# Kernel tuning notes

Hardware: AMD Instinct MI355X
Metric: run time of the kernel (lower is better)

The kernel has to match this reference:

```python
import jax, jax.numpy as jnp
import numpy as np

B = 16      # number of graphs (equal-sized, batch = repeat(arange(B), N))


def _knn_edges(pos, k, total):
    """Batch-aware kNN graph, torch_geometric knn_graph semantics.

    loop=False, flow='source_to_target': for each query node i, its k nearest
    neighbors j produce edges (row=j neighbor/source, col=i query/target).
    Returns (row, col) as flat global int32 index arrays of length B*N*k.
    """
    N = total // B
    posb = pos.reshape(B, N, -1)                      # [B, N, 3]
    sq = jnp.sum(posb * posb, axis=-1)                # [B, N]
    # squared Euclidean distances, [B, N, N]
    d2 = sq[:, :, None] + sq[:, None, :] - 2.0 * jnp.einsum('bnd,bmd->bnm', posb, posb)
    d2 = jnp.where(jnp.eye(N, dtype=bool)[None], jnp.inf, d2)  # exclude self-loops
    _, nbr = jax.lax.top_k(-d2, k)                    # [B, N, k] local neighbor idx
    offs = (jnp.arange(B, dtype=nbr.dtype) * N)[:, None, None]
    row = (nbr + offs).reshape(-1)                                      # neighbors (sources)
    col = jnp.broadcast_to(jnp.arange(N, dtype=nbr.dtype)[None, :, None] + offs,
                           (B, N, k)).reshape(-1)                       # query nodes (targets)
    return row, col


def reference(x, pos, batch, k):
    total = x.shape[0]
    row, col = _knn_edges(pos, k, total)
    # scatter_mean(x[col], row, dim_size=total): mean of gathered features per row index
    sums = jax.ops.segment_sum(x[col], row, num_segments=total)          # [total, d]
    cnt = jax.ops.segment_sum(jnp.ones(row.shape, x.dtype), row, num_segments=total)
    x_neigh_mean = sums / jnp.maximum(cnt, 1.0)[:, None]                 # empty rows -> 0
    return jnp.sum(jnp.abs(x - x_neigh_mean), axis=-1)                   # L1 norm, [total]


def setup_inputs() -> dict:
    key = jax.random.key(0)
    k1, k2 = jax.random.split(key)
    N = 4096
    x = jax.random.normal(k1, (B * N, 64), dtype=jnp.float32)
    pos = jax.random.normal(k2, (B * N, 3), dtype=jnp.float32)
    batch = jnp.repeat(jnp.arange(B, dtype=jnp.int64), N)
    return {"x": x, "pos": pos, "batch": batch, "k": 10}
```

## Files before the change

### kernel.cpp

```cpp
#include <hip/hip_runtime.h>
#include <stdint.h>

#define NB 16
#define NN 4096
#define KK 10
#define NL 11
#define FD 64
#define TOTAL (NB * NN)
#define NW 8
#define CH 512
#define SOCT 32
#define QG 64
#define PCAP 64
#define PPITCH 129

typedef float f2 __attribute__((ext_vector_type(2)));

#define INFF __int_as_float(0x7f800000)

__device__ __forceinline__ f2 d2pair(f2 nmx, f2 nmy, f2 nmz, f2 sqi2,
                                     float4 A, float4 B) {
#pragma clang fp contract(off)
    f2 cx = {A.x, A.y}, cy = {A.z, A.w};
    f2 cz = {B.x, B.y}, cw = {B.z, B.w};
    f2 t = nmx * cx + nmy * cy;
    f2 nd = t + nmz * cz;
    nd = nd + nd;
    f2 s = sqi2 + cw;
    return s + nd;
}

__device__ __forceinline__ uint32_t d2exact(float mx, float my, float mz, float sqi,
                                            float cx, float cy, float cz, float cw) {
    float dot = __fadd_rn(__fadd_rn(__fmul_rn(mx, cx), __fmul_rn(my, cy)),
                          __fmul_rn(mz, cz));
    float d2 = __fsub_rn(__fadd_rn(sqi, cw), __fmul_rn(2.0f, dot));
    return __float_as_uint(d2);
}

__global__ __launch_bounds__(256) void prep_kernel(const float* __restrict__ pos,
                                                   float4* __restrict__ pp4,
                                                   int* __restrict__ cnt) {
    const int p = blockIdx.x * 256 + threadIdx.x;
    const float* s = pos + (size_t)p * 6;
    float x0 = s[0], y0 = s[1], z0 = s[2];
    float x1 = s[3], y1 = s[4], z1 = s[5];
    float q0 = __fadd_rn(__fadd_rn(__fmul_rn(x0, x0), __fmul_rn(y0, y0)),
                         __fmul_rn(z0, z0));
    float q1 = __fadd_rn(__fadd_rn(__fmul_rn(x1, x1), __fmul_rn(y1, y1)),
                         __fmul_rn(z1, z1));
    pp4[2 * p + 0] = make_float4(x0, x1, y0, y1);
    pp4[2 * p + 1] = make_float4(z0, z1, q0, q1);
    cnt[2 * p + 0] = 0;
    cnt[2 * p + 1] = 0;
}

__global__ __launch_bounds__(512, 8) void knn_kernel(const float4* __restrict__ pp4,
                                                     int* __restrict__ cnt,
                                                     int* __restrict__ colfix,
                                                     int* __restrict__ nbr) {
    __shared__ uint32_t pool[QG * PPITCH];
    __shared__ float tau_s[QG];
    __shared__ unsigned int qcnt[QG];
    float* poolf = (float*)pool;

    const int tid = threadIdx.x;
    const int lane = tid & 63;
    const int w = __builtin_amdgcn_readfirstlane(tid >> 6);
    const int batch = blockIdx.x >> 6;
    const int qloc = ((blockIdx.x & 63) << 6) | lane;
    const int gbase = batch << 12;
    const int gq = gbase + qloc;

    float4 mA = pp4[(gq >> 1) * 2 + 0];
    float4 mB = pp4[(gq >> 1) * 2 + 1];
    const bool hi = (qloc & 1);
    const float mx = hi ? mA.y : mA.x;
    const float my = hi ? mA.w : mA.z;
    const float mz = hi ? mB.y : mB.x;
    const float sqi = hi ? mB.w : mB.z;
    const f2 nmx = {-mx, -mx}, nmy = {-my, -my}, nmz = {-mz, -mz};
    const f2 sqi2 = {sqi, sqi};

    const float4* __restrict__ cp = pp4 + (size_t)(gbase + w * CH);

    float L[NL];
#pragma unroll
    for (int t = 0; t < NL; t++) L[t] = INFF;

#pragma unroll 2
    for (int o = 0; o < SOCT; ++o) {
        const float4* cb = cp + o * 8;
        f2 d0 = d2pair(nmx, nmy, nmz, sqi2, cb[0], cb[1]);
        f2 d1 = d2pair(nmx, nmy, nmz, sqi2, cb[2], cb[3]);
        f2 d2v = d2pair(nmx, nmy, nmz, sqi2, cb[4], cb[5]);
        f2 d3 = d2pair(nmx, nmy, nmz, sqi2, cb[6], cb[7]);
        float m0 = fminf(d0.x, d0.y), m1 = fminf(d1.x, d1.y);
        float m2 = fminf(d2v.x, d2v.y), m3 = fminf(d3.x, d3.y);
        float m = fminf(fminf(m0, m1), fminf(m2, m3));
#pragma unroll
        for (int t = 0; t < NL - 1; ++t) L[t] = __builtin_amdgcn_fmed3f(L[t], L[t + 1], m);
        L[NL - 1] = fminf(L[NL - 1], m);
    }
#pragma unroll
    for (int t = 0; t < NL; t++) poolf[tid * NL + t] = L[t];
    if (tid < QG) qcnt[tid] = 0u;
    __syncthreads();

    if (tid < QG) {
        int p[NW];
#pragma unroll
        for (int u = 0; u < NW; u++) p[u] = NL - 1;
        float tau = INFF;
        for (int it = 0; it < NL; ++it) {
            float best = INFF;
            int bw = 0;
#pragma unroll
            for (int u = 0; u < NW; u++) {
                float v = (p[u] >= 0) ? poolf[(u * QG + tid) * NL + p[u]] : INFF;
                if (v < best) { best = v; bw = u; }
            }
            p[bw]--;
            tau = best;
        }
        tau_s[tid] = tau;
    }
    __syncthreads();

    const float tau = tau_s[lane];
#pragma unroll 2
    for (int pi = 0; pi < CH / 2; ++pi) {
        f2 d = d2pair(nmx, nmy, nmz, sqi2, cp[2 * pi], cp[2 * pi + 1]);
        if (fminf(d.x, d.y) <= tau) {
            if (d.x <= tau) {
                unsigned pp = atomicAdd(&qcnt[lane], 1u);
                if (pp < PCAP) pool[lane * PPITCH + 2 * pp + 1] = (uint32_t)(w * CH + 2 * pi);
            }
            if (d.y <= tau) {
                unsigned pp = atomicAdd(&qcnt[lane], 1u);
                if (pp < PCAP) pool[lane * PPITCH + 2 * pp + 1] = (uint32_t)(w * CH + 2 * pi + 1);
            }
        }
    }
    __syncthreads();

    if (tid < QG) {
        uint64_t S[KK];
#pragma unroll
        for (int t = 0; t < KK; t++) S[t] = ~0ull;
        unsigned R = qcnt[tid];
        if (R > PCAP) R = PCAP;
        for (unsigned e = 0; e < R; ++e) {
            uint32_t ix = pool[tid * PPITCH + 2 * e + 1];
            if (ix == (uint32_t)qloc) continue;
            int g = gbase + (int)ix;
            float4 A = pp4[(g >> 1) * 2 + 0];
            float4 B = pp4[(g >> 1) * 2 + 1];
            bool ch = (ix & 1);
            uint32_t db = d2exact(mx, my, mz, sqi,
                                  ch ? A.y : A.x, ch ? A.w : A.z,
                                  ch ? B.y : B.x, ch ? B.w : B.z);
            uint64_t k64 = ((uint64_t)db << 32) | ix;
            if (k64 < S[0]) {
                bool sh[KK];
                sh[0] = true;
#pragma unroll
                for (int t = 1; t < KK; t++) sh[t] = (k64 < S[t]);
#pragma unroll
                for (int t = 0; t < KK; t++) {
                    uint64_t vac = sh[t] ? k64 : S[t];
                    S[t] = (t + 1 < KK) ? (sh[t + 1] ? S[t + 1] : vac) : vac;
                }
            }
        }
#pragma unroll
        for (int t = 0; t < KK; t++) {
            int jl = (int)(S[t] & 0xffffffffu);
            int gj = gbase + jl;
            int p = atomicAdd(&cnt[gj], 1);
            if (colfix) {
                if (p < 64) colfix[(gj << 6) | p] = gq;
            } else {
                nbr[gq * KK + t] = gj;
            }
        }
    }
}

__global__ __launch_bounds__(256) void out_bucket_kernel(const float4* __restrict__ x4,
                                                         const int* __restrict__ colfix,
                                                         const int* __restrict__ cnt,
                                                         float* __restrict__ out) {
    const int gid = blockIdx.x * 256 + threadIdx.x;
    const int n = gid >> 4;
    const int s = gid & 15;
    const int c = cnt[n];
    const int cc = (c > 64) ? 64 : c;
    const int base = n << 6;
    float4 acc = make_float4(0.f, 0.f, 0.f, 0.f);
    int e = 0;
    for (; e + 2 <= cc; e += 2) {
        int q0 = colfix[base + e], q1 = colfix[base + e + 1];
        float4 v0 = x4[(q0 << 4) | s];
        float4 v1 = x4[(q1 << 4) | s];
        acc.x += v0.x; acc.y += v0.y; acc.z += v0.z; acc.w += v0.w;
        acc.x += v1.x; acc.y += v1.y; acc.z += v1.z; acc.w += v1.w;
    }
    if (e < cc) {
        int q0 = colfix[base + e];
        float4 v0 = x4[(q0 << 4) | s];
        acc.x += v0.x; acc.y += v0.y; acc.z += v0.z; acc.w += v0.w;
    }
    const float inv = 1.0f / (float)(c > 1 ? c : 1);
    float4 mn = x4[(n << 4) | s];
    float v = fabsf(mn.x - acc.x * inv) + fabsf(mn.y - acc.y * inv) +
              fabsf(mn.z - acc.z * inv) + fabsf(mn.w - acc.w * inv);
    v += __shfl_xor(v, 1, 64);
    v += __shfl_xor(v, 2, 64);
    v += __shfl_xor(v, 4, 64);
    v += __shfl_xor(v, 8, 64);
    if (s == 0) out[n] = v;
}

__global__ __launch_bounds__(1024) void scan_kernel(const int* __restrict__ cnt,
                                                    int* __restrict__ offs) {
    __shared__ int lds[1024];
    const int t = threadIdx.x;
    const int base = t * 64;
    int s = 0;
    for (int i = 0; i < 64; i++) s += cnt[base + i];
    lds[t] = s;
    __syncthreads();
    for (int off = 1; off < 1024; off <<= 1) {
        int v = (t >= off) ? lds[t - off] : 0;
        __syncthreads();
        lds[t] += v;
        __syncthreads();
    }
    int run = lds[t] - s;
    for (int i = 0; i < 64; i++) {
        offs[base + i] = run;
        run += cnt[base + i];
    }
}

__global__ __launch_bounds__(256) void fill_kernel(const int* __restrict__ nbr,
                                                   int* __restrict__ offs,
                                                   int* __restrict__ col) {
    const int i = blockIdx.x * 256 + threadIdx.x;
#pragma unroll
    for (int t = 0; t < KK; t++) {
        int j = nbr[i * KK + t];
        int p = atomicAdd(&offs[j], 1);
        col[p] = i;
    }
}

__global__ __launch_bounds__(256) void out_kernel(const float* __restrict__ x,
                                                  const int* __restrict__ col,
                                                  const int* __restrict__ offs_end,
                                                  const int* __restrict__ cnt,
                                                  float* __restrict__ out) {
    const int gtid = blockIdx.x * 256 + threadIdx.x;
    const int n = gtid >> 6;
    const int lane = gtid & 63;
    const int c = cnt[n];
    const int end = offs_end[n];
    const int start = end - c;
    float s = 0.0f;
    for (int e = start; e < end; e++) {
        int i = col[e];
        s += x[(size_t)i * FD + lane];
    }
    float mean = s / (float)(c > 1 ? c : 1);
    float v = fabsf(x[(size_t)n * FD + lane] - mean);
#pragma unroll
    for (int off = 32; off; off >>= 1) v += __shfl_xor(v, off, 64);
    if (lane == 0) out[n] = v;
}

extern "C" void kernel_launch(void* const* d_in, const int* in_sizes, int n_in,
                              void* d_out, int out_size, void* d_ws, size_t ws_size,
                              hipStream_t stream) {
    const float* x = (const float*)d_in[0];
    const float* pos = (const float*)d_in[1];
    float* out = (float*)d_out;

    char* ws = (char*)d_ws;
    float4* pp4 = (float4*)(ws + 0);
    int* cnt = (int*)(ws + 1048576);
    int* colfix = (int*)(ws + 1310720);
    int* nbr = (int*)(ws + 1310720);
    int* offs = (int*)(ws + 3932160);
    int* col = (int*)(ws + 4194304);

    const bool bucket = ws_size >= (size_t)(1310720 + TOTAL * 64 * 4);

    hipLaunchKernelGGL(prep_kernel, dim3(TOTAL / 2 / 256), dim3(256), 0, stream, pos, pp4, cnt);
    hipLaunchKernelGGL(knn_kernel, dim3(TOTAL / QG), dim3(512), 0, stream, pp4, cnt,
                       bucket ? colfix : (int*)nullptr, bucket ? (int*)nullptr : nbr);
    if (bucket) {
        hipLaunchKernelGGL(out_bucket_kernel, dim3(TOTAL * 16 / 256), dim3(256), 0, stream,
                           (const float4*)x, colfix, cnt, out);
    } else {
        hipLaunchKernelGGL(scan_kernel, dim3(1), dim3(1024), 0, stream, cnt, offs);
        hipLaunchKernelGGL(fill_kernel, dim3(TOTAL / 256), dim3(256), 0, stream, nbr, offs, col);
        hipLaunchKernelGGL(out_kernel, dim3(TOTAL * FD / 256), dim3(256), 0, stream,
                           x, col, offs, cnt, out);
    }
}
```

Measured before the change: 216.7 us.

## Replace shared LDS atomic candidate pool with per-wave uint16 lists and FMA distances

```diff
diff --git a/kernel.cpp b/kernel.cpp
--- a/kernel.cpp
+++ b/kernel.cpp
@@ -11,23 +11,14 @@
 #define CH 512
 #define SOCT 32
 #define QG 64
-#define PCAP 64
-#define PPITCH 129
-
-typedef float f2 __attribute__((ext_vector_type(2)));
+#define WCAP 24
+#define WPITCH 25
 
 #define INFF __int_as_float(0x7f800000)
 
-__device__ __forceinline__ f2 d2pair(f2 nmx, f2 nmy, f2 nmz, f2 sqi2,
-                                     float4 A, float4 B) {
-#pragma clang fp contract(off)
-    f2 cx = {A.x, A.y}, cy = {A.z, A.w};
-    f2 cz = {B.x, B.y}, cw = {B.z, B.w};
-    f2 t = nmx * cx + nmy * cy;
-    f2 nd = t + nmz * cz;
-    nd = nd + nd;
-    f2 s = sqi2 + cw;
-    return s + nd;
+__device__ __forceinline__ float Fd2(float cx, float cy, float cz, float cq,
+                                     float vx2, float vy2, float vz2, float sqi) {
+    return __fmaf_rn(vz2, cz, __fmaf_rn(vy2, cy, __fmaf_rn(vx2, cx, __fadd_rn(sqi, cq))));
 }
 
 __device__ __forceinline__ uint32_t d2exact(float mx, float my, float mz, float sqi,
@@ -59,10 +50,11 @@
                                                      int* __restrict__ cnt,
                                                      int* __restrict__ colfix,
                                                      int* __restrict__ nbr) {
-    __shared__ uint32_t pool[QG * PPITCH];
+    __shared__ uint32_t smem[6400];
     __shared__ float tau_s[QG];
-    __shared__ unsigned int qcnt[QG];
-    float* poolf = (float*)pool;
+    __shared__ uint32_t qcntw[QG * NW];
+    float* listf = (float*)smem;
+    uint16_t* pool16 = (uint16_t*)smem;
 
     const int tid = threadIdx.x;
     const int lane = tid & 63;
@@ -79,10 +71,23 @@
     const float my = hi ? mA.w : mA.z;
     const float mz = hi ? mB.y : mB.x;
     const float sqi = hi ? mB.w : mB.z;
-    const f2 nmx = {-mx, -mx}, nmy = {-my, -my}, nmz = {-mz, -mz};
-    const f2 sqi2 = {sqi, sqi};
+    const float vx2 = __fmul_rn(-2.0f, mx);
+    const float vy2 = __fmul_rn(-2.0f, my);
+    const float vz2 = __fmul_rn(-2.0f, mz);
 
     const float4* __restrict__ cp = pp4 + (size_t)(gbase + w * CH);
+
+#define D8(cb)                                                        \
+    float4 A0 = (cb)[0], B0 = (cb)[1], A1 = (cb)[2], B1 = (cb)[3];    \
+    float4 A2 = (cb)[4], B2 = (cb)[5], A3 = (cb)[6], B3 = (cb)[7];    \
+    float d0 = Fd2(A0.x, A0.z, B0.x, B0.z, vx2, vy2, vz2, sqi);       \
+    float d1 = Fd2(A0.y, A0.w, B0.y, B0.w, vx2, vy2, vz2, sqi);       \
+    float d2 = Fd2(A1.x, A1.z, B1.x, B1.z, vx2, vy2, vz2, sqi);       \
+    float d3 = Fd2(A1.y, A1.w, B1.y, B1.w, vx2, vy2, vz2, sqi);       \
+    float d4 = Fd2(A2.x, A2.z, B2.x, B2.z, vx2, vy2, vz2, sqi);       \
+    float d5 = Fd2(A2.y, A2.w, B2.y, B2.w, vx2, vy2, vz2, sqi);       \
+    float d6 = Fd2(A3.x, A3.z, B3.x, B3.z, vx2, vy2, vz2, sqi);       \
+    float d7 = Fd2(A3.y, A3.w, B3.y, B3.w, vx2, vy2, vz2, sqi);
 
     float L[NL];
 #pragma unroll
@@ -91,20 +96,15 @@
 #pragma unroll 2
     for (int o = 0; o < SOCT; ++o) {
         const float4* cb = cp + o * 8;
-        f2 d0 = d2pair(nmx, nmy, nmz, sqi2, cb[0], cb[1]);
-        f2 d1 = d2pair(nmx, nmy, nmz, sqi2, cb[2], cb[3]);
-        f2 d2v = d2pair(nmx, nmy, nmz, sqi2, cb[4], cb[5]);
-        f2 d3 = d2pair(nmx, nmy, nmz, sqi2, cb[6], cb[7]);
-        float m0 = fminf(d0.x, d0.y), m1 = fminf(d1.x, d1.y);
-        float m2 = fminf(d2v.x, d2v.y), m3 = fminf(d3.x, d3.y);
-        float m = fminf(fminf(m0, m1), fminf(m2, m3));
+        D8(cb);
+        float m = fminf(fminf(fminf(d0, d1), fminf(d2, d3)),
+                        fminf(fminf(d4, d5), fminf(d6, d7)));
 #pragma unroll
         for (int t = 0; t < NL - 1; ++t) L[t] = __builtin_amdgcn_fmed3f(L[t], L[t + 1], m);
         L[NL - 1] = fminf(L[NL - 1], m);
     }
 #pragma unroll
-    for (int t = 0; t < NL; t++) poolf[tid * NL + t] = L[t];
-    if (tid < QG) qcnt[tid] = 0u;
+    for (int t = 0; t < NL; t++) listf[tid * NL + t] = L[t];
     __syncthreads();
 
     if (tid < QG) {
@@ -117,7 +117,7 @@
             int bw = 0;
 #pragma unroll
             for (int u = 0; u < NW; u++) {
-                float v = (p[u] >= 0) ? poolf[(u * QG + tid) * NL + p[u]] : INFF;
+                float v = (p[u] >= 0) ? listf[((u << 6) | tid) * NL + p[u]] : INFF;
                 if (v < best) { best = v; bw = u; }
             }
             p[bw]--;
@@ -127,49 +127,54 @@
     }
     __syncthreads();
 
-    const float tau = tau_s[lane];
-#pragma unroll 2
-    for (int pi = 0; pi < CH / 2; ++pi) {
-        f2 d = d2pair(nmx, nmy, nmz, sqi2, cp[2 * pi], cp[2 * pi + 1]);
-        if (fminf(d.x, d.y) <= tau) {
-            if (d.x <= tau) {
-                unsigned pp = atomicAdd(&qcnt[lane], 1u);
-                if (pp < PCAP) pool[lane * PPITCH + 2 * pp + 1] = (uint32_t)(w * CH + 2 * pi);
-            }
-            if (d.y <= tau) {
-                unsigned pp = atomicAdd(&qcnt[lane], 1u);
-                if (pp < PCAP) pool[lane * PPITCH + 2 * pp + 1] = (uint32_t)(w * CH + 2 * pi + 1);
-            }
+    const float tau = tau_s[lane] * 1.00001f;
+    const uint32_t cell0 = (uint32_t)((lane * NW + w) * WPITCH);
+    uint32_t cpos = cell0;
+    for (int o = 0; o < CH / 8; ++o) {
+        const float4* cb = cp + o * 8;
+        D8(cb);
+        const uint32_t jb = (uint32_t)(w * CH + o * 8);
+#define PUSH(dv, off)                                              \
+        if ((dv) <= tau && cpos < cell0 + WCAP) {                  \
+            pool16[cpos] = (uint16_t)(jb + (off));                 \
+            cpos++;                                                \
         }
-    }
+        PUSH(d0, 0) PUSH(d1, 1) PUSH(d2, 2) PUSH(d3, 3)
+        PUSH(d4, 4) PUSH(d5, 5) PUSH(d6, 6) PUSH(d7, 7)
+#undef PUSH
+    }
+    qcntw[lane * NW + w] = cpos - cell0;
     __syncthreads();
 
     if (tid < QG) {
         uint64_t S[KK];
 #pragma unroll
         for (int t = 0; t < KK; t++) S[t] = ~0ull;
-        unsigned R = qcnt[tid];
-        if (R > PCAP) R = PCAP;
-        for (unsigned e = 0; e < R; ++e) {
-            uint32_t ix = pool[tid * PPITCH + 2 * e + 1];
-            if (ix == (uint32_t)qloc) continue;
-            int g = gbase + (int)ix;
-            float4 A = pp4[(g >> 1) * 2 + 0];
-            float4 B = pp4[(g >> 1) * 2 + 1];
-            bool ch = (ix & 1);
-            uint32_t db = d2exact(mx, my, mz, sqi,
-                                  ch ? A.y : A.x, ch ? A.w : A.z,
-                                  ch ? B.y : B.x, ch ? B.w : B.z);
-            uint64_t k64 = ((uint64_t)db << 32) | ix;
-            if (k64 < S[0]) {
-                bool sh[KK];
-                sh[0] = true;
-#pragma unroll
-                for (int t = 1; t < KK; t++) sh[t] = (k64 < S[t]);
-#pragma unroll
-                for (int t = 0; t < KK; t++) {
-                    uint64_t vac = sh[t] ? k64 : S[t];
-                    S[t] = (t + 1 < KK) ? (sh[t + 1] ? S[t + 1] : vac) : vac;
+#pragma unroll
+        for (int u = 0; u < NW; u++) {
+            uint32_t c2 = qcntw[tid * NW + u];
+            const uint16_t* st = pool16 + (tid * NW + u) * WPITCH;
+            for (uint32_t e = 0; e < c2; ++e) {
+                uint32_t ix = st[e];
+                if (ix == (uint32_t)qloc) continue;
+                int g = gbase + (int)ix;
+                float4 A = pp4[(g >> 1) * 2 + 0];
+                float4 B = pp4[(g >> 1) * 2 + 1];
+                bool ch = (ix & 1);
+                uint32_t db = d2exact(mx, my, mz, sqi,
+                                      ch ? A.y : A.x, ch ? A.w : A.z,
+                                      ch ? B.y : B.x, ch ? B.w : B.z);
+                uint64_t k64 = ((uint64_t)db << 32) | ix;
+                if (k64 < S[0]) {
+                    bool sh[KK];
+                    sh[0] = true;
+#pragma unroll
+                    for (int t = 1; t < KK; t++) sh[t] = (k64 < S[t]);
+#pragma unroll
+                    for (int t = 0; t < KK; t++) {
+                        uint64_t vac = sh[t] ? k64 : S[t];
+                        S[t] = (t + 1 < KK) ? (sh[t + 1] ? S[t + 1] : vac) : vac;
+                    }
                 }
             }
         }
@@ -185,6 +190,7 @@
             }
         }
     }
+#undef D8
 }
 
 __global__ __launch_bounds__(256) void out_bucket_kernel(const float4* __restrict__ x4,
```

Measured after the change: 202.4 us. 1.07x faster.
